# Kernel tuning notes

Hardware: AMD Instinct MI355X
Metric: run time of the kernel (lower is better)

## Reference

```python
import jax, jax.numpy as jnp
import numpy as np

N_NODES = 50000
N_EDGES = 800000
NEG_SLOPE = 0.2  # GATConv default
BN_EPS = 1e-5


def _seg_softmax(logits, seg, n):
    # per-target-node softmax over incoming edges (PyG softmax w/ +1e-16)
    m = jax.ops.segment_max(logits, seg, num_segments=n)
    m = jnp.where(jnp.isfinite(m), m, 0.0)
    e = jnp.exp(logits - m[seg])
    s = jax.ops.segment_sum(e, seg, num_segments=n)
    return e / (s[seg] + 1e-16)


def _gat_conv(x, src, dst, W, a_src, a_dst, b, concat):
    # x: [N, Fin]; W: [Fin, H*C]; a_src/a_dst: [H, C]
    n = x.shape[0]
    H, C = a_src.shape
    h = (x @ W).reshape(n, H, C)
    al_s = jnp.einsum('nhc,hc->nh', h, a_src)
    al_d = jnp.einsum('nhc,hc->nh', h, a_dst)
    logits = jax.nn.leaky_relu(al_s[src] + al_d[dst], NEG_SLOPE)  # [E, H]
    alpha = _seg_softmax(logits, dst, n)                           # [E, H]
    out = jax.ops.segment_sum(h[src] * alpha[:, :, None], dst, num_segments=n)
    out = out.reshape(n, H * C) if concat else out.mean(axis=1)
    return out + b


def _bn(x, g, b):
    mu = jnp.mean(x, axis=0)
    var = jnp.mean((x - mu) ** 2, axis=0)
    return (x - mu) * jax.lax.rsqrt(var + BN_EPS) * g + b


def _gat_params(key, fin, heads, ch, scale=0.1):
    k1, k2, k3 = jax.random.split(key, 3)
    W = jax.random.normal(k1, (fin, heads * ch), jnp.float32) * scale
    a_s = jax.random.normal(k2, (heads, ch), jnp.float32) * scale
    a_d = jax.random.normal(k3, (heads, ch), jnp.float32) * scale
    return W, a_s, a_d


def setup_inputs() -> dict:
    key = jax.random.key(0)
    ks = jax.random.split(key, 12)
    inp = {}
    inp['x'] = jax.random.normal(ks[0], (N_NODES, 3), jnp.float32)
    inp['edge_index'] = jax.random.randint(ks[1], (2, N_EDGES), 0, N_NODES, jnp.int64 if jax.config.jax_enable_x64 else jnp.int32)
    inp['W11'], inp['as11'], inp['ad11'] = _gat_params(ks[2], 3, 8, 8)
    inp['b11'] = jnp.zeros((64,), jnp.float32)
    inp['W12'], inp['as12'], inp['ad12'] = _gat_params(ks[3], 64, 8, 8)
    inp['b12'] = jnp.zeros((64,), jnp.float32)
    inp['g1'] = jnp.ones((64,), jnp.float32)
    inp['be1'] = jnp.zeros((64,), jnp.float32)
    inp['W21'], inp['as21'], inp['ad21'] = _gat_params(ks[4], 64, 8, 32)
    inp['b21'] = jnp.zeros((256,), jnp.float32)
    inp['W22'], inp['as22'], inp['ad22'] = _gat_params(ks[5], 256, 8, 32)
    inp['b22'] = jnp.zeros((256,), jnp.float32)
    inp['g2'] = jnp.ones((256,), jnp.float32)
    inp['be2'] = jnp.zeros((256,), jnp.float32)
    inp['W31'], inp['as31'], inp['ad31'] = _gat_params(ks[6], 256, 8, 64)
    inp['b31'] = jnp.zeros((512,), jnp.float32)
    inp['W32'], inp['as32'], inp['ad32'] = _gat_params(ks[7], 512, 8, 1)
    inp['b32'] = jnp.zeros((1,), jnp.float32)
    return inp


def reference(x, edge_index,
              W11, as11, ad11, b11, W12, as12, ad12, b12, g1, be1,
              W21, as21, ad21, b21, W22, as22, ad22, b22, g2, be2,
              W31, as31, ad31, b31, W32, as32, ad32, b32):
    n = x.shape[0]
    loops = jnp.arange(n, dtype=edge_index.dtype)
    src = jnp.concatenate([edge_index[0], loops])  # add_self_loops=True
    dst = jnp.concatenate([edge_index[1], loops])
    # GAT(3, 64, 2): conv -> relu -> conv
    h = jax.nn.relu(_gat_conv(x, src, dst, W11, as11, ad11, b11, True))
    h = _gat_conv(h, src, dst, W12, as12, ad12, b12, True)
    h = jax.nn.leaky_relu(_bn(h, g1, be1), 0.1)
    # GAT(64, 256, 2)
    h = jax.nn.relu(_gat_conv(h, src, dst, W21, as21, ad21, b21, True))
    h = _gat_conv(h, src, dst, W22, as22, ad22, b22, True)
    h = jax.nn.leaky_relu(_bn(h, g2, be2), 0.1)
    # GAT(256, 512, 2, 1): conv -> relu -> conv(concat=False)
    h = jax.nn.relu(_gat_conv(h, src, dst, W31, as31, ad31, b31, True))
    h = _gat_conv(h, src, dst, W32, as32, ad32, b32, False)
    return jax.nn.sigmoid(h)
```

## Files before the change

kernel.cpp:

```cpp
#include <hip/hip_runtime.h>
#include <math.h>

typedef short short8 __attribute__((ext_vector_type(8)));
typedef short short4v __attribute__((ext_vector_type(4)));
typedef float f32x4 __attribute__((ext_vector_type(4)));

__device__ __forceinline__ unsigned short f2bf(float v){
  unsigned u = __builtin_bit_cast(unsigned, v);
  u += 0x7FFFu + ((u >> 16) & 1u);
  return (unsigned short)(u >> 16);
}
__device__ __forceinline__ float bf2f(unsigned short b){
  unsigned u = ((unsigned)b) << 16;
  return __builtin_bit_cast(float, u);
}

__global__ void k_deg(const int* __restrict__ dstv, int* __restrict__ deg, int E){
  int e = blockIdx.x*blockDim.x + threadIdx.x;
  if (e < E) atomicAdd(&deg[dstv[e]], 1);
}

__global__ void k_scan(const int* __restrict__ deg, int* __restrict__ off,
                       int* __restrict__ cursor, int N){
  __shared__ int wpre[16];
  __shared__ int s_tot;
  __shared__ int carry;
  int tid = threadIdx.x;
  int lane = tid & 63, wv = tid >> 6;
  if (tid == 0) carry = 0;
  __syncthreads();
  for (int base = 0; base < N; base += 1024){
    int i = base + tid;
    int v = (i < N) ? deg[i] : 0;
    int incl = v;
    #pragma unroll
    for (int d = 1; d < 64; d <<= 1){
      int t = __shfl_up(incl, d, 64);
      if (lane >= d) incl += t;
    }
    if (lane == 63) wpre[wv] = incl;
    __syncthreads();
    if (tid < 16){
      int x = wpre[tid];
      int ix = x;
      #pragma unroll
      for (int d = 1; d < 16; d <<= 1){
        int t = __shfl_up(ix, d, 16);
        if (tid >= d) ix += t;
      }
      wpre[tid] = ix - x;
      if (tid == 15) s_tot = ix;
    }
    __syncthreads();
    int c = carry;
    int excl = c + wpre[wv] + (incl - v);
    if (i < N){ off[i+1] = excl + v; cursor[i] = excl; }
    __syncthreads();
    if (tid == 0) carry = c + s_tot;
    __syncthreads();
  }
  if (tid == 0) off[0] = 0;
}

__global__ void k_fill(const int* __restrict__ srcv, const int* __restrict__ dstv,
                       int* __restrict__ cursor, int* __restrict__ csr, int E){
  int e = blockIdx.x*blockDim.x + threadIdx.x;
  if (e < E){
    int d = dstv[e];
    int p = atomicAdd(&cursor[d], 1);
    csr[p] = srcv[e];
  }
}

__global__ void k_prepB(const float* __restrict__ W, unsigned short* __restrict__ bh,
                        unsigned short* __restrict__ bl, int K, int kpshift, int Nn){
  int Kp = 1 << kpshift;
  int i = blockIdx.x*blockDim.x + threadIdx.x;
  if (i >= Nn*Kp) return;
  int n = i >> kpshift, k = i & (Kp-1);
  float v = (k < K) ? W[(size_t)k*Nn + n] : 0.0f;
  unsigned short h = f2bf(v);
  bh[i] = h;
  bl[i] = f2bf(v - bf2f(h));
}

__global__ void k_bn_coef(const float* __restrict__ bsum, const float* __restrict__ bsq,
                          const float* __restrict__ g, const float* __restrict__ b,
                          float* __restrict__ sc, float* __restrict__ sh,
                          float invN, int HC){
  int f = threadIdx.x + blockIdx.x*blockDim.x;
  if (f >= HC) return;
  float mu  = bsum[f]*invN;
  float var = bsq[f]*invN - mu*mu;
  float rs  = rsqrtf(var + 1e-5f) * g[f];
  sc[f] = rs;
  sh[f] = b[f] - mu*rs;
}

template<int BN, int AFMT>
__global__ __launch_bounds__((BN==64)?256:512)
void gemm_mfma(const void* __restrict__ Av, const unsigned short* __restrict__ Bh,
               const unsigned short* __restrict__ Bl,
               const float* __restrict__ bnsc, const float* __restrict__ bnsh,
               const float* __restrict__ a_s, const float* __restrict__ a_d,
               unsigned short* __restrict__ Pb, float* __restrict__ Ds,
               float* __restrict__ Dd, int M, int K){
  constexpr int WAVES   = (BN==64) ? 4 : 8;
  constexpr int BLOCK   = WAVES*64;
  constexpr int WAVES_N = BN/64;
  constexpr int WAVES_M = WAVES/WAVES_N;
  constexpr int WM      = 64/WAVES_M;
  constexpr int MF      = WM/16;
  constexpr int CH      = (BN==512)?64 : (BN==256)?32 : 8;
  constexpr int TERMS   = (AFMT==2) ? 2 : 3;
  const int Kp = (K + 63) & ~(int)63;

  __shared__ char lds[(TERMS==3)?16384:8192];

  int tid  = threadIdx.x;
  int lane = tid & 63;
  int wid  = tid >> 6;
  int wn = wid % WAVES_N;
  int wm = wid / WAVES_N;
  int n0w = wn*64;
  int wm0 = wm*WM;
  int m0 = blockIdx.x * 64;

  f32x4 acc[MF][4];
  #pragma unroll
  for (int i = 0; i < MF; ++i)
    #pragma unroll
    for (int j = 0; j < 4; ++j)
      acc[i][j] = (f32x4){0.f,0.f,0.f,0.f};

  constexpr int SITER = 512/BLOCK;

  for (int k0 = 0; k0 < Kp; k0 += 64){
    __syncthreads();
    #pragma unroll
    for (int it = 0; it < SITER; ++it){
      int i = it*BLOCK + tid;
      int row = i >> 3, c8 = i & 7;
      int gm = m0 + row;
      int gk = k0 + c8*8;
      int off = row*128 + ((c8 ^ (row&7))<<4);
      if constexpr (AFMT == 2){
        short8 hv = {0,0,0,0,0,0,0,0};
        if (gm < M) hv = *(const short8*)((const unsigned short*)Av + (size_t)gm*K + gk);
        *(short8*)(lds + off) = hv;
      } else if constexpr (AFMT == 1){
        short8 raw = {0,0,0,0,0,0,0,0};
        if (gm < M) raw = *(const short8*)((const unsigned short*)Av + (size_t)gm*K + gk);
        short8 hi, lo;
        #pragma unroll
        for (int j=0;j<8;++j){
          float u = bf2f((unsigned short)raw[j])*bnsc[gk+j] + bnsh[gk+j];
          u = u > 0.f ? u : 0.1f*u;
          if (gm >= M) u = 0.f;
          unsigned short hb = f2bf(u);
          hi[j] = (short)hb;
          lo[j] = (short)f2bf(u - bf2f(hb));
        }
        *(short8*)(lds + off) = hi;
        *(short8*)(lds + 8192 + off) = lo;
      } else {
        const float* A = (const float*)Av;
        float v[8];
        if (gm < M && gk + 8 <= K){
          const float* ap = A + (size_t)gm*K + gk;
          float4 x0 = *(const float4*)ap;
          float4 x1 = *(const float4*)(ap+4);
          v[0]=x0.x; v[1]=x0.y; v[2]=x0.z; v[3]=x0.w;
          v[4]=x1.x; v[5]=x1.y; v[6]=x1.z; v[7]=x1.w;
        } else {
          #pragma unroll
          for (int j=0;j<8;++j){
            int gkj = gk + j;
            v[j] = (gm < M && gkj < K) ? A[(size_t)gm*K + gkj] : 0.0f;
          }
        }
        short8 hi, lo;
        #pragma unroll
        for (int j=0;j<8;++j){
          unsigned short hb = f2bf(v[j]);
          hi[j] = (short)hb;
          lo[j] = (short)f2bf(v[j] - bf2f(hb));
        }
        *(short8*)(lds + off) = hi;
        *(short8*)(lds + 8192 + off) = lo;
      }
    }
    __syncthreads();
    #pragma unroll
    for (int kk = 0; kk < 2; ++kk){
      short8 bhf[4], blf[4];
      #pragma unroll
      for (int nf = 0; nf < 4; ++nf){
        int ncol = n0w + nf*16 + (lane & 15);
        int kidx = k0 + kk*32 + ((lane>>4)<<3);
        size_t bo = (size_t)ncol*Kp + kidx;
        bhf[nf] = *(const short8*)(Bh + bo);
        blf[nf] = *(const short8*)(Bl + bo);
      }
      #pragma unroll
      for (int mt = 0; mt < MF; ++mt){
        int row = wm0 + mt*16 + (lane & 15);
        int c8 = kk*4 + (lane>>4);
        int off = row*128 + ((c8 ^ (row&7))<<4);
        short8 ah = *(const short8*)(lds + off);
        #pragma unroll
        for (int nf = 0; nf < 4; ++nf){
          acc[mt][nf] = __builtin_amdgcn_mfma_f32_16x16x32_bf16(ah, bhf[nf], acc[mt][nf], 0,0,0);
          acc[mt][nf] = __builtin_amdgcn_mfma_f32_16x16x32_bf16(ah, blf[nf], acc[mt][nf], 0,0,0);
        }
        if constexpr (TERMS == 3){
          short8 al = *(const short8*)(lds + 8192 + off);
          #pragma unroll
          for (int nf = 0; nf < 4; ++nf)
            acc[mt][nf] = __builtin_amdgcn_mfma_f32_16x16x32_bf16(al, bhf[nf], acc[mt][nf], 0,0,0);
        }
      }
    }
  }

  float asv[4], adv[4];
  #pragma unroll
  for (int nf=0; nf<4; ++nf){
    int gcol = n0w + nf*16 + (lane&15);
    asv[nf] = a_s[gcol];
    adv[nf] = a_d[gcol];
  }
  #pragma unroll
  for (int mt = 0; mt < MF; ++mt){
    #pragma unroll
    for (int r = 0; r < 4; ++r){
      int gm = m0 + wm0 + mt*16 + ((lane>>4)<<2) + r;
      bool ok = gm < M;
      #pragma unroll
      for (int nf=0;nf<4;++nf){
        if (ok) Pb[(size_t)gm*BN + n0w + nf*16 + (lane&15)] = f2bf(acc[mt][nf][r]);
      }
      if constexpr (CH == 64){
        float ps = acc[mt][0][r]*asv[0] + acc[mt][1][r]*asv[1]
                 + acc[mt][2][r]*asv[2] + acc[mt][3][r]*asv[3];
        float pd = acc[mt][0][r]*adv[0] + acc[mt][1][r]*adv[1]
                 + acc[mt][2][r]*adv[2] + acc[mt][3][r]*adv[3];
        #pragma unroll
        for (int d2=1; d2<16; d2<<=1){ ps += __shfl_xor(ps,d2,64); pd += __shfl_xor(pd,d2,64); }
        if (ok && (lane&15)==0){
          int head = n0w >> 6;
          Ds[(size_t)gm*8 + head] = ps;
          Dd[(size_t)gm*8 + head] = pd;
        }
      } else if constexpr (CH == 32){
        float ps0 = acc[mt][0][r]*asv[0] + acc[mt][1][r]*asv[1];
        float ps1 = acc[mt][2][r]*asv[2] + acc[mt][3][r]*asv[3];
        float pd0 = acc[mt][0][r]*adv[0] + acc[mt][1][r]*adv[1];
        float pd1 = acc[mt][2][r]*adv[2] + acc[mt][3][r]*adv[3];
        #pragma unroll
        for (int d2=1; d2<16; d2<<=1){
          ps0 += __shfl_xor(ps0,d2,64); ps1 += __shfl_xor(ps1,d2,64);
          pd0 += __shfl_xor(pd0,d2,64); pd1 += __shfl_xor(pd1,d2,64);
        }
        if (ok && (lane&15)==0){
          int head = n0w >> 5;
          Ds[(size_t)gm*8 + head]     = ps0;
          Ds[(size_t)gm*8 + head + 1] = ps1;
          Dd[(size_t)gm*8 + head]     = pd0;
          Dd[(size_t)gm*8 + head + 1] = pd1;
        }
      } else {
        #pragma unroll
        for (int nf=0;nf<4;++nf){
          float ps = acc[mt][nf][r]*asv[nf];
          float pd = acc[mt][nf][r]*adv[nf];
          #pragma unroll
          for (int d2=1; d2<8; d2<<=1){ ps += __shfl_xor(ps,d2,64); pd += __shfl_xor(pd,d2,64); }
          if (ok && (lane&7)==0){
            int head = nf*2 + ((lane>>3)&1);
            Ds[(size_t)gm*8 + head] = ps;
            Dd[(size_t)gm*8 + head] = pd;
          }
        }
      }
    }
  }
}

template<int HC, int ACT>
__global__ __launch_bounds__(256)
void k_agg(const unsigned short* __restrict__ Pb, const float* __restrict__ Ds,
           const float* __restrict__ Dd, const int* __restrict__ off,
           const int* __restrict__ csr, const float* __restrict__ bias,
           unsigned short* __restrict__ outb, int N){
  constexpr int R = HC/64;
  __shared__ float salpha[4][512];
  int lane = threadIdx.x & 63;
  int wid  = threadIdx.x >> 6;
  int n = blockIdx.x*4 + wid;
  if (n >= N) return;
  int o0 = off[n], deg = off[n+1]-o0;
  int myh = lane >> 3;

  float aldn[8];
  {
    const float* dn = Dd + (size_t)n*8;
    float4 x0 = *(const float4*)dn;
    float4 x1 = *(const float4*)(dn+4);
    aldn[0]=x0.x; aldn[1]=x0.y; aldn[2]=x0.z; aldn[3]=x0.w;
    aldn[4]=x1.x; aldn[5]=x1.y; aldn[6]=x1.z; aldn[7]=x1.w;
  }

  float acc[R];
  #pragma unroll
  for (int j=0;j<R;++j) acc[j]=0.f;

  if (deg < 64){
    int nE = deg + 1;
    int myidx = (lane < deg) ? csr[o0+lane] : n;
    bool active = (lane < nE);
    float v[8];
    {
      const float* dp = Ds + (size_t)myidx*8;
      float4 x0 = *(const float4*)dp;
      float4 x1 = *(const float4*)(dp+4);
      float t[8] = {x0.x,x0.y,x0.z,x0.w,x1.x,x1.y,x1.z,x1.w};
      #pragma unroll
      for (int h=0;h<8;++h){
        float u = t[h] + aldn[h];
        u = u > 0.f ? u : 0.2f*u;
        v[h] = active ? u : -1e30f;
      }
    }
    float m[8];
    #pragma unroll
    for (int h=0;h<8;++h) m[h]=v[h];
    #pragma unroll
    for (int d=1; d<64; d<<=1)
      #pragma unroll
      for (int h=0;h<8;++h) m[h] = fmaxf(m[h], __shfl_xor(m[h], d, 64));
    float sv[8], s[8];
    #pragma unroll
    for (int h=0;h<8;++h){ sv[h] = active ? __expf(v[h]-m[h]) : 0.f; s[h]=sv[h]; }
    #pragma unroll
    for (int d=1; d<64; d<<=1)
      #pragma unroll
      for (int h=0;h<8;++h) s[h] += __shfl_xor(s[h], d, 64);
    if (active){
      #pragma unroll
      for (int h=0;h<8;++h) salpha[wid][lane*8+h] = sv[h] / (s[h] + 1e-16f);
    }
    asm volatile("s_waitcnt lgkmcnt(0)" ::: "memory");

    for (int e=0; e<nE; ++e){
      int src = __shfl(myidx, e, 64);
      float alpha = salpha[wid][e*8 + myh];
      const unsigned short* hp = Pb + (size_t)src*HC + lane*R;
      if constexpr (R == 1){
        acc[0] += alpha * bf2f(hp[0]);
      } else if constexpr (R == 4){
        short4v w = *(const short4v*)hp;
        #pragma unroll
        for (int j=0;j<4;++j) acc[j] += alpha * bf2f((unsigned short)w[j]);
      } else {
        short8 w = *(const short8*)hp;
        #pragma unroll
        for (int j=0;j<8;++j) acc[j] += alpha * bf2f((unsigned short)w[j]);
      }
    }
  } else {
    float m[8];
    #pragma unroll
    for (int h=0;h<8;++h) m[h] = -1e30f;
    for (int e = lane; e <= deg; e += 64){
      int src = (e < deg) ? csr[o0+e] : n;
      const float* ap = Ds + (size_t)src*8;
      #pragma unroll
      for (int h=0;h<8;++h){
        float u = ap[h] + aldn[h];
        u = u > 0.f ? u : 0.2f*u;
        m[h] = fmaxf(m[h], u);
      }
    }
    #pragma unroll
    for (int d=1; d<64; d<<=1)
      #pragma unroll
      for (int h=0;h<8;++h) m[h] = fmaxf(m[h], __shfl_xor(m[h], d, 64));
    float s[8] = {0,0,0,0,0,0,0,0};
    for (int e = lane; e <= deg; e += 64){
      int src = (e < deg) ? csr[o0+e] : n;
      const float* ap = Ds + (size_t)src*8;
      #pragma unroll
      for (int h=0;h<8;++h){
        float u = ap[h] + aldn[h];
        u = u > 0.f ? u : 0.2f*u;
        s[h] += __expf(u - m[h]);
      }
    }
    #pragma unroll
    for (int d=1; d<64; d<<=1)
      #pragma unroll
      for (int h=0;h<8;++h) s[h] += __shfl_xor(s[h], d, 64);
    float mh = m[myh];
    float rsh = 1.0f/(s[myh] + 1e-16f);
    float adh = aldn[myh];
    for (int e = 0; e <= deg; ++e){
      int src = (e < deg) ? csr[o0+e] : n;
      float u = Ds[(size_t)src*8 + myh] + adh;
      u = u > 0.f ? u : 0.2f*u;
      float alpha = __expf(u - mh) * rsh;
      const unsigned short* hp = Pb + (size_t)src*HC + lane*R;
      if constexpr (R == 1){
        acc[0] += alpha * bf2f(hp[0]);
      } else if constexpr (R == 4){
        short4v w = *(const short4v*)hp;
        #pragma unroll
        for (int j=0;j<4;++j) acc[j] += alpha * bf2f((unsigned short)w[j]);
      } else {
        short8 w = *(const short8*)hp;
        #pragma unroll
        for (int j=0;j<8;++j) acc[j] += alpha * bf2f((unsigned short)w[j]);
      }
    }
  }

  #pragma unroll
  for (int j = 0; j < R; ++j){
    int f = lane*R + j;
    float v = acc[j] + bias[f];
    if (ACT == 1) v = fmaxf(v, 0.0f);
    outb[(size_t)n*HC + f] = f2bf(v);
  }
}

__global__ void k_bn_stats(const unsigned short* __restrict__ x, float* __restrict__ gsum,
                           float* __restrict__ gsq, int N, int HC){
  int f = threadIdx.x;
  float s = 0.f, q = 0.f;
  for (int r = blockIdx.x; r < N; r += gridDim.x){
    float v = bf2f(x[(size_t)r*HC + f]);
    s += v; q += v*v;
  }
  atomicAdd(&gsum[f], s);
  atomicAdd(&gsq[f], q);
}

__global__ __launch_bounds__(256)
void gemm8(const unsigned short* __restrict__ Qb, const float* __restrict__ W,
           float* __restrict__ h8, int M){
  int lane = threadIdx.x & 63;
  int gw = (blockIdx.x*blockDim.x + threadIdx.x) >> 6;
  int nw = (gridDim.x*blockDim.x) >> 6;
  float w[8][8];
  const float* wp = W + lane*64;
  #pragma unroll
  for (int j=0;j<8;++j){
    float4 a = *(const float4*)(wp + j*8);
    float4 b = *(const float4*)(wp + j*8 + 4);
    w[j][0]=a.x; w[j][1]=a.y; w[j][2]=a.z; w[j][3]=a.w;
    w[j][4]=b.x; w[j][5]=b.y; w[j][6]=b.z; w[j][7]=b.w;
  }
  for (int n = gw; n < M; n += nw){
    short8 v8 = *(const short8*)(Qb + (size_t)n*512 + lane*8);
    float p[8] = {0,0,0,0,0,0,0,0};
    #pragma unroll
    for (int j=0;j<8;++j){
      float x = bf2f((unsigned short)v8[j]);
      #pragma unroll
      for (int o=0;o<8;++o) p[o] += x * w[j][o];
    }
    #pragma unroll
    for (int d=1; d<64; d<<=1)
      #pragma unroll
      for (int o=0;o<8;++o) p[o] += __shfl_xor(p[o], d, 64);
    if (lane == 0){
      float4 y0 = make_float4(p[0],p[1],p[2],p[3]);
      float4 y1 = make_float4(p[4],p[5],p[6],p[7]);
      *(float4*)(h8 + (size_t)n*8)     = y0;
      *(float4*)(h8 + (size_t)n*8 + 4) = y1;
    }
  }
}

__global__ __launch_bounds__(256)
void k_final(const float* __restrict__ h8, const float* __restrict__ a_s,
             const float* __restrict__ a_d, const int* __restrict__ off,
             const int* __restrict__ csr, const float* __restrict__ b32,
             float* __restrict__ outp, int N){
  int lane = threadIdx.x & 63;
  int wv   = threadIdx.x >> 6;
  int n = blockIdx.x*4 + wv;
  if (n >= N) return;
  int o0 = off[n], deg = off[n+1]-o0;
  float asv[8], adv[8];
  #pragma unroll
  for (int h=0;h<8;++h){ asv[h]=a_s[h]; adv[h]=a_d[h]; }
  float aldn[8];
  {
    const float* hp = h8 + (size_t)n*8;
    float4 x0 = *(const float4*)hp;
    float4 x1 = *(const float4*)(hp+4);
    float hn[8] = {x0.x,x0.y,x0.z,x0.w,x1.x,x1.y,x1.z,x1.w};
    #pragma unroll
    for (int h=0;h<8;++h) aldn[h] = hn[h]*adv[h];
  }

  if (deg < 64){
    int nE = deg + 1;
    int src = (lane < deg) ? csr[o0+lane] : n;
    bool act = (lane < nE);
    float hs[8];
    {
      const float* hp = h8 + (size_t)src*8;
      float4 x0 = *(const float4*)hp;
      float4 x1 = *(const float4*)(hp+4);
      hs[0]=x0.x; hs[1]=x0.y; hs[2]=x0.z; hs[3]=x0.w;
      hs[4]=x1.x; hs[5]=x1.y; hs[6]=x1.z; hs[7]=x1.w;
    }
    float v[8];
    #pragma unroll
    for (int h=0;h<8;++h){
      float u = hs[h]*asv[h] + aldn[h];
      u = u > 0.f ? u : 0.2f*u;
      v[h] = act ? u : -1e30f;
    }
    float m[8];
    #pragma unroll
    for (int h=0;h<8;++h) m[h]=v[h];
    #pragma unroll
    for (int d=1; d<64; d<<=1)
      #pragma unroll
      for (int h=0;h<8;++h) m[h] = fmaxf(m[h], __shfl_xor(m[h], d, 64));
    float s[8], t[8];
    #pragma unroll
    for (int h=0;h<8;++h){
      float e = act ? __expf(v[h]-m[h]) : 0.f;
      s[h]=e; t[h]=e*hs[h];
    }
    #pragma unroll
    for (int d=1; d<64; d<<=1)
      #pragma unroll
      for (int h=0;h<8;++h){
        s[h] += __shfl_xor(s[h], d, 64);
        t[h] += __shfl_xor(t[h], d, 64);
      }
    if (lane == 0){
      float o = 0.f;
      #pragma unroll
      for (int h=0;h<8;++h) o += t[h]/(s[h]+1e-16f);
      o = o*0.125f + b32[0];
      outp[n] = 1.0f/(1.0f + __expf(-o));
    }
  } else if (lane == 0){
    float m[8], s[8], agg[8];
    #pragma unroll
    for (int h=0;h<8;++h){ m[h]=-1e30f; s[h]=0.f; agg[h]=0.f; }
    for (int e = 0; e <= deg; ++e){
      int src = (e < deg) ? csr[o0+e] : n;
      #pragma unroll
      for (int h=0;h<8;++h){
        float u = h8[(size_t)src*8+h]*asv[h] + aldn[h];
        u = u > 0.f ? u : 0.2f*u;
        m[h] = fmaxf(m[h], u);
      }
    }
    for (int e = 0; e <= deg; ++e){
      int src = (e < deg) ? csr[o0+e] : n;
      #pragma unroll
      for (int h=0;h<8;++h){
        float u = h8[(size_t)src*8+h]*asv[h] + aldn[h];
        u = u > 0.f ? u : 0.2f*u;
        float ex = __expf(u - m[h]);
        s[h] += ex;
        agg[h] += ex * h8[(size_t)src*8+h];
      }
    }
    float o = 0.f;
    #pragma unroll
    for (int h=0;h<8;++h) o += agg[h]/(s[h]+1e-16f);
    o = o*0.125f + b32[0];
    outp[n] = 1.0f/(1.0f + __expf(-o));
  }
}

extern "C" void kernel_launch(void* const* d_in, const int* in_sizes, int n_in,
                              void* d_out, int out_size, void* d_ws, size_t ws_size,
                              hipStream_t stream){
  int N = in_sizes[0]/3;
  int E = in_sizes[1]/2;
  const float* x    = (const float*)d_in[0];
  const int*   ei   = (const int*)  d_in[1];
  const float* W11  = (const float*)d_in[2];
  const float* as11 = (const float*)d_in[3];
  const float* ad11 = (const float*)d_in[4];
  const float* b11  = (const float*)d_in[5];
  const float* W12  = (const float*)d_in[6];
  const float* as12 = (const float*)d_in[7];
  const float* ad12 = (const float*)d_in[8];
  const float* b12  = (const float*)d_in[9];
  const float* g1   = (const float*)d_in[10];
  const float* be1  = (const float*)d_in[11];
  const float* W21  = (const float*)d_in[12];
  const float* as21 = (const float*)d_in[13];
  const float* ad21 = (const float*)d_in[14];
  const float* b21  = (const float*)d_in[15];
  const float* W22  = (const float*)d_in[16];
  const float* as22 = (const float*)d_in[17];
  const float* ad22 = (const float*)d_in[18];
  const float* b22  = (const float*)d_in[19];
  const float* g2   = (const float*)d_in[20];
  const float* be2  = (const float*)d_in[21];
  const float* W31  = (const float*)d_in[22];
  const float* as31 = (const float*)d_in[23];
  const float* ad31 = (const float*)d_in[24];
  const float* b31  = (const float*)d_in[25];
  const float* W32  = (const float*)d_in[26];
  const float* as32 = (const float*)d_in[27];
  const float* ad32 = (const float*)d_in[28];
  const float* b32  = (const float*)d_in[29];

  char* ws = (char*)d_ws;
  size_t o = 0;
  auto alloc = [&](size_t bytes)->char*{
    char* p = ws + o;
    o = (o + bytes + 255) & ~(size_t)255;
    return p;
  };
  int*   deg    = (int*)  alloc((size_t)N*4);
  int*   off    = (int*)  alloc((size_t)(N+1)*4);
  int*   cursor = (int*)  alloc((size_t)N*4);
  int*   csr    = (int*)  alloc((size_t)E*4);
  unsigned short* bth = (unsigned short*)alloc(131072*2);
  unsigned short* btl = (unsigned short*)alloc(131072*2);
  float* h8     = (float*)alloc((size_t)N*8*4);
  float* bsum   = (float*)alloc(1024);
  float* bsq    = (float*)alloc(1024);
  float* bnsc   = (float*)alloc(1024);
  float* bnsh   = (float*)alloc(1024);
  unsigned short* Pb = (unsigned short*)alloc((size_t)N*512*2);
  unsigned short* Qb = (unsigned short*)alloc((size_t)N*512*2);
  float* Dsb    = (float*)alloc((size_t)N*8*4);
  float* Ddb    = (float*)alloc((size_t)N*8*4);
  (void)ws_size;

  hipMemsetAsync(deg, 0, (size_t)N*4, stream);
  int eb = (E+255)/256;
  k_deg <<<eb, 256, 0, stream>>>(ei+E, deg, E);
  k_scan<<<1, 1024, 0, stream>>>(deg, off, cursor, N);
  k_fill<<<eb, 256, 0, stream>>>(ei, ei+E, cursor, csr, E);

  int mb = (N+63)/64;
  int nb4 = (N+3)/4;
  float invN = 1.0f/(float)N;

  k_prepB<<<(64*64)/256, 256, 0, stream>>>(W11, bth, btl, 3, 6, 64);
  gemm_mfma<64,0><<<mb, 256, 0, stream>>>(x, bth, btl, nullptr, nullptr,
                                          as11, ad11, Pb, Dsb, Ddb, N, 3);
  k_agg<64,1><<<nb4, 256, 0, stream>>>(Pb, Dsb, Ddb, off, csr, b11, Qb, N);

  k_prepB<<<(64*64)/256, 256, 0, stream>>>(W12, bth, btl, 64, 6, 64);
  gemm_mfma<64,2><<<mb, 256, 0, stream>>>(Qb, bth, btl, nullptr, nullptr,
                                          as12, ad12, Pb, Dsb, Ddb, N, 64);
  k_agg<64,0><<<nb4, 256, 0, stream>>>(Pb, Dsb, Ddb, off, csr, b12, Qb, N);
  hipMemsetAsync(bsum, 0, 2048, stream);
  k_bn_stats<<<512, 64, 0, stream>>>(Qb, bsum, bsq, N, 64);
  k_bn_coef<<<1, 64, 0, stream>>>(bsum, bsq, g1, be1, bnsc, bnsh, invN, 64);

  k_prepB<<<(256*64)/256, 256, 0, stream>>>(W21, bth, btl, 64, 6, 256);
  gemm_mfma<256,1><<<mb, 512, 0, stream>>>(Qb, bth, btl, bnsc, bnsh,
                                           as21, ad21, Pb, Dsb, Ddb, N, 64);
  k_agg<256,1><<<nb4, 256, 0, stream>>>(Pb, Dsb, Ddb, off, csr, b21, Qb, N);

  k_prepB<<<(256*256)/256, 256, 0, stream>>>(W22, bth, btl, 256, 8, 256);
  gemm_mfma<256,2><<<mb, 512, 0, stream>>>(Qb, bth, btl, nullptr, nullptr,
                                           as22, ad22, Pb, Dsb, Ddb, N, 256);
  k_agg<256,0><<<nb4, 256, 0, stream>>>(Pb, Dsb, Ddb, off, csr, b22, Qb, N);
  hipMemsetAsync(bsum, 0, 2048, stream);
  k_bn_stats<<<512, 256, 0, stream>>>(Qb, bsum, bsq, N, 256);
  k_bn_coef<<<1, 256, 0, stream>>>(bsum, bsq, g2, be2, bnsc, bnsh, invN, 256);

  k_prepB<<<(512*256)/256, 256, 0, stream>>>(W31, bth, btl, 256, 8, 512);
  gemm_mfma<512,1><<<mb, 512, 0, stream>>>(Qb, bth, btl, bnsc, bnsh,
                                           as31, ad31, Pb, Dsb, Ddb, N, 256);
  k_agg<512,1><<<nb4, 256, 0, stream>>>(Pb, Dsb, Ddb, off, csr, b31, Qb, N);

  gemm8<<<1024, 256, 0, stream>>>(Qb, W32, h8, N);
  k_final<<<nb4, 256, 0, stream>>>(h8, as32, ad32, off, csr, b32,
                                   (float*)d_out, N);
}
```

Measured before the change: 1.140 ms.

## Batch weight prep, use atomic-free BN partials, and unroll edge gather in aggregation

Five per-layer weight-split kernels become one launch that writes every layer's bf16 hi/lo weights into a combined buffer at fixed offsets. BN statistics now store per-block partial sums that the coef kernel reduces, which removes the float atomics and the memsets. The low-degree aggregation loop is unrolled by 4 or 8 edges with independent accumulators, so several gathers are in flight at once, and it uses 32-bit index math. This cuts launch count and memory latency stalls, at the cost of more registers in k_agg and a serial 128-row loop in k_bn_coef.

```diff
diff --git a/kernel.cpp b/kernel.cpp
--- a/kernel.cpp
+++ b/kernel.cpp
@@ -72,26 +72,49 @@
   }
 }
 
-__global__ void k_prepB(const float* __restrict__ W, unsigned short* __restrict__ bh,
-                        unsigned short* __restrict__ bl, int K, int kpshift, int Nn){
-  int Kp = 1 << kpshift;
+__global__ void k_prepAll(const float* __restrict__ W11, const float* __restrict__ W12,
+                          const float* __restrict__ W21, const float* __restrict__ W22,
+                          const float* __restrict__ W31,
+                          unsigned short* __restrict__ bh, unsigned short* __restrict__ bl){
   int i = blockIdx.x*blockDim.x + threadIdx.x;
-  if (i >= Nn*Kp) return;
-  int n = i >> kpshift, k = i & (Kp-1);
+  if (i >= 221184) return;
+  const float* W; int K, kpsh, off, Nn;
+  if (i < 4096)       { W=W11; K=3;   kpsh=6; off=0;     Nn=64;  }
+  else if (i < 8192)  { W=W12; K=64;  kpsh=6; off=4096;  Nn=64;  }
+  else if (i < 24576) { W=W21; K=64;  kpsh=6; off=8192;  Nn=256; }
+  else if (i < 90112) { W=W22; K=256; kpsh=8; off=24576; Nn=256; }
+  else                { W=W31; K=256; kpsh=8; off=90112; Nn=512; }
+  int j = i - off;
+  int Kp = 1 << kpsh;
+  int n = j >> kpsh, k = j & (Kp-1);
   float v = (k < K) ? W[(size_t)k*Nn + n] : 0.0f;
   unsigned short h = f2bf(v);
   bh[i] = h;
   bl[i] = f2bf(v - bf2f(h));
 }
 
-__global__ void k_bn_coef(const float* __restrict__ bsum, const float* __restrict__ bsq,
+__global__ void k_bn_stats(const unsigned short* __restrict__ x, float* __restrict__ psum,
+                           float* __restrict__ psq, int N, int HC){
+  int f = threadIdx.x;
+  float s = 0.f, q = 0.f;
+  for (int r = blockIdx.x; r < N; r += gridDim.x){
+    float v = bf2f(x[(size_t)r*HC + f]);
+    s += v; q += v*v;
+  }
+  psum[blockIdx.x*HC + f] = s;
+  psq [blockIdx.x*HC + f] = q;
+}
+
+__global__ void k_bn_coef(const float* __restrict__ psum, const float* __restrict__ psq,
                           const float* __restrict__ g, const float* __restrict__ b,
                           float* __restrict__ sc, float* __restrict__ sh,
-                          float invN, int HC){
+                          float invN, int HC, int nb){
   int f = threadIdx.x + blockIdx.x*blockDim.x;
   if (f >= HC) return;
-  float mu  = bsum[f]*invN;
-  float var = bsq[f]*invN - mu*mu;
+  float s = 0.f, q = 0.f;
+  for (int r = 0; r < nb; ++r){ s += psum[r*HC+f]; q += psq[r*HC+f]; }
+  float mu  = s*invN;
+  float var = q*invN - mu*mu;
   float rs  = rsqrtf(var + 1e-5f) * g[f];
   sc[f] = rs;
   sh[f] = b[f] - mu*rs;
@@ -294,6 +317,7 @@
            const int* __restrict__ csr, const float* __restrict__ bias,
            unsigned short* __restrict__ outb, int N){
   constexpr int R = HC/64;
+  constexpr int UF = (R==1) ? 8 : 4;
   __shared__ float salpha[4][512];
   int lane = threadIdx.x & 63;
   int wid  = threadIdx.x >> 6;
@@ -304,7 +328,7 @@
 
   float aldn[8];
   {
-    const float* dn = Dd + (size_t)n*8;
+    const float* dn = Dd + (unsigned)n*8u;
     float4 x0 = *(const float4*)dn;
     float4 x1 = *(const float4*)(dn+4);
     aldn[0]=x0.x; aldn[1]=x0.y; aldn[2]=x0.z; aldn[3]=x0.w;
@@ -321,7 +345,7 @@
     bool active = (lane < nE);
     float v[8];
     {
-      const float* dp = Ds + (size_t)myidx*8;
+      const float* dp = Ds + (unsigned)myidx*8u;
       float4 x0 = *(const float4*)dp;
       float4 x1 = *(const float4*)(dp+4);
       float t[8] = {x0.x,x0.y,x0.z,x0.w,x1.x,x1.y,x1.z,x1.w};
@@ -352,21 +376,62 @@
     }
     asm volatile("s_waitcnt lgkmcnt(0)" ::: "memory");
 
-    for (int e=0; e<nE; ++e){
-      int src = __shfl(myidx, e, 64);
+    const unsigned short* Pl = Pb + lane*R;
+    float accu[UF][R];
+    #pragma unroll
+    for (int u=0;u<UF;++u)
+      #pragma unroll
+      for (int j=0;j<R;++j) accu[u][j] = 0.f;
+
+    int e = 0;
+    #pragma unroll 1
+    for (; e + UF <= nE; e += UF){
+      unsigned bse[UF];
+      float av[UF];
+      #pragma unroll
+      for (int u=0;u<UF;++u){
+        int sidx = __shfl(myidx, e+u, 64);
+        bse[u] = (unsigned)sidx * (unsigned)HC;
+        av[u]  = salpha[wid][(e+u)*8 + myh];
+      }
+      #pragma unroll
+      for (int u=0;u<UF;++u){
+        if constexpr (R == 1){
+          accu[u][0] += av[u] * bf2f(Pl[bse[u]]);
+        } else if constexpr (R == 4){
+          short4v w = *(const short4v*)(Pl + bse[u]);
+          #pragma unroll
+          for (int j=0;j<4;++j) accu[u][j] += av[u] * bf2f((unsigned short)w[j]);
+        } else {
+          short8 w = *(const short8*)(Pl + bse[u]);
+          #pragma unroll
+          for (int j=0;j<8;++j) accu[u][j] += av[u] * bf2f((unsigned short)w[j]);
+        }
+      }
+    }
+    #pragma unroll 1
+    for (; e < nE; ++e){
+      int sidx = __shfl(myidx, e, 64);
+      unsigned bs = (unsigned)sidx * (unsigned)HC;
       float alpha = salpha[wid][e*8 + myh];
-      const unsigned short* hp = Pb + (size_t)src*HC + lane*R;
       if constexpr (R == 1){
-        acc[0] += alpha * bf2f(hp[0]);
+        accu[0][0] += alpha * bf2f(Pl[bs]);
       } else if constexpr (R == 4){
-        short4v w = *(const short4v*)hp;
-        #pragma unroll
-        for (int j=0;j<4;++j) acc[j] += alpha * bf2f((unsigned short)w[j]);
+        short4v w = *(const short4v*)(Pl + bs);
+        #pragma unroll
+        for (int j=0;j<4;++j) accu[0][j] += alpha * bf2f((unsigned short)w[j]);
       } else {
-        short8 w = *(const short8*)hp;
-        #pragma unroll
-        for (int j=0;j<8;++j) acc[j] += alpha * bf2f((unsigned short)w[j]);
-      }
+        short8 w = *(const short8*)(Pl + bs);
+        #pragma unroll
+        for (int j=0;j<8;++j) accu[0][j] += alpha * bf2f((unsigned short)w[j]);
+      }
+    }
+    #pragma unroll
+    for (int j=0;j<R;++j){
+      float t0 = 0.f;
+      #pragma unroll
+      for (int u=0;u<UF;++u) t0 += accu[u][j];
+      acc[j] = t0;
     }
   } else {
     float m[8];
@@ -431,18 +496,6 @@
     if (ACT == 1) v = fmaxf(v, 0.0f);
     outb[(size_t)n*HC + f] = f2bf(v);
   }
-}
-
-__global__ void k_bn_stats(const unsigned short* __restrict__ x, float* __restrict__ gsum,
-                           float* __restrict__ gsq, int N, int HC){
-  int f = threadIdx.x;
-  float s = 0.f, q = 0.f;
-  for (int r = blockIdx.x; r < N; r += gridDim.x){
-    float v = bf2f(x[(size_t)r*HC + f]);
-    s += v; q += v*v;
-  }
-  atomicAdd(&gsum[f], s);
-  atomicAdd(&gsq[f], q);
 }
 
 __global__ __launch_bounds__(256)
@@ -630,11 +683,11 @@
   int*   off    = (int*)  alloc((size_t)(N+1)*4);
   int*   cursor = (int*)  alloc((size_t)N*4);
   int*   csr    = (int*)  alloc((size_t)E*4);
-  unsigned short* bth = (unsigned short*)alloc(131072*2);
-  unsigned short* btl = (unsigned short*)alloc(131072*2);
+  unsigned short* bh = (unsigned short*)alloc(221184*2);
+  unsigned short* bl = (unsigned short*)alloc(221184*2);
   float* h8     = (float*)alloc((size_t)N*8*4);
-  float* bsum   = (float*)alloc(1024);
-  float* bsq    = (float*)alloc(1024);
+  float* psum   = (float*)alloc(128*256*4);
+  float* psq    = (float*)alloc(128*256*4);
   float* bnsc   = (float*)alloc(1024);
   float* bnsh   = (float*)alloc(1024);
   unsigned short* Pb = (unsigned short*)alloc((size_t)N*512*2);
@@ -643,9 +696,12 @@
   float* Ddb    = (float*)alloc((size_t)N*8*4);
   (void)ws_size;
 
+  const int BT11=0, BT12=4096, BT21=8192, BT22=24576, BT31=90112;
+
   hipMemsetAsync(deg, 0, (size_t)N*4, stream);
   int eb = (E+255)/256;
   k_deg <<<eb, 256, 0, stream>>>(ei+E, deg, E);
+  k_prepAll<<<(221184+255)/256, 256, 0, stream>>>(W11, W12, W21, W22, W31, bh, bl);
   k_scan<<<1, 1024, 0, stream>>>(deg, off, cursor, N);
   k_fill<<<eb, 256, 0, stream>>>(ei, ei+E, cursor, csr, E);
 
@@ -653,34 +709,27 @@
   int nb4 = (N+3)/4;
   float invN = 1.0f/(float)N;
 
-  k_prepB<<<(64*64)/256, 256, 0, stream>>>(W11, bth, btl, 3, 6, 64);
-  gemm_mfma<64,0><<<mb, 256, 0, stream>>>(x, bth, btl, nullptr, nullptr,
+  gemm_mfma<64,0><<<mb, 256, 0, stream>>>(x, bh+BT11, bl+BT11, nullptr, nullptr,
                                           as11, ad11, Pb, Dsb, Ddb, N, 3);
   k_agg<64,1><<<nb4, 256, 0, stream>>>(Pb, Dsb, Ddb, off, csr, b11, Qb, N);
 
-  k_prepB<<<(64*64)/256, 256, 0, stream>>>(W12, bth, btl, 64, 6, 64);
-  gemm_mfma<64,2><<<mb, 256, 0, stream>>>(Qb, bth, btl, nullptr, nullptr,
+  gemm_mfma<64,2><<<mb, 256, 0, stream>>>(Qb, bh+BT12, bl+BT12, nullptr, nullptr,
                                           as12, ad12, Pb, Dsb, Ddb, N, 64);
   k_agg<64,0><<<nb4, 256, 0, stream>>>(Pb, Dsb, Ddb, off, csr, b12, Qb, N);
-  hipMemsetAsync(bsum, 0, 2048, stream);
-  k_bn_stats<<<512, 64, 0, stream>>>(Qb, bsum, bsq, N, 64);
-  k_bn_coef<<<1, 64, 0, stream>>>(bsum, bsq, g1, be1, bnsc, bnsh, invN, 64);
-
-  k_prepB<<<(256*64)/256, 256, 0, stream>>>(W21, bth, btl, 64, 6, 256);
-  gemm_mfma<256,1><<<mb, 512, 0, stream>>>(Qb, bth, btl, bnsc, bnsh,
+  k_bn_stats<<<128, 64, 0, stream>>>(Qb, psum, psq, N, 64);
+  k_bn_coef<<<1, 64, 0, stream>>>(psum, psq, g1, be1, bnsc, bnsh, invN, 64, 128);
+
+  gemm_mfma<256,1><<<mb, 512, 0, stream>>>(Qb, bh+BT21, bl+BT21, bnsc, bnsh,
                                            as21, ad21, Pb, Dsb, Ddb, N, 64);
   k_agg<256,1><<<nb4, 256, 0, stream>>>(Pb, Dsb, Ddb, off, csr, b21, Qb, N);
 
-  k_prepB<<<(256*256)/256, 256, 0, stream>>>(W22, bth, btl, 256, 8, 256);
-  gemm_mfma<256,2><<<mb, 512, 0, stream>>>(Qb, bth, btl, nullptr, nullptr,
+  gemm_mfma<256,2><<<mb, 512, 0, stream>>>(Qb, bh+BT22, bl+BT22, nullptr, nullptr,
                                            as22, ad22, Pb, Dsb, Ddb, N, 256);
   k_agg<256,0><<<nb4, 256, 0, stream>>>(Pb, Dsb, Ddb, off, csr, b22, Qb, N);
-  hipMemsetAsync(bsum, 0, 2048, stream);
-  k_bn_stats<<<512, 256, 0, stream>>>(Qb, bsum, bsq, N, 256);
-  k_bn_coef<<<1, 256, 0, stream>>>(bsum, bsq, g2, be2, bnsc, bnsh, invN, 256);
-
-  k_prepB<<<(512*256)/256, 256, 0, stream>>>(W31, bth, btl, 256, 8, 512);
-  gemm_mfma<512,1><<<mb, 512, 0, stream>>>(Qb, bth, btl, bnsc, bnsh,
+  k_bn_stats<<<128, 256, 0, stream>>>(Qb, psum, psq, N, 256);
+  k_bn_coef<<<1, 256, 0, stream>>>(psum, psq, g2, be2, bnsc, bnsh, invN, 256, 128);
+
+  gemm_mfma<512,1><<<mb, 512, 0, stream>>>(Qb, bh+BT31, bl+BT31, bnsc, bnsh,
                                            as31, ad31, Pb, Dsb, Ddb, N, 256);
   k_agg<512,1><<<nb4, 256, 0, stream>>>(Pb, Dsb, Ddb, off, csr, b31, Qb, N);
 
```

New measurement: 1.270 ms. 1.11x slower.
